# Performance work log

Measured on AMD Instinct MI355X. Metric: run time of the kernel, lower is better.

The kernel has to match this reference:

```python
import jax, jax.numpy as jnp
import numpy as np

NUM_ITEMS = 100000
N = NUM_ITEMS + 1
D = 64
H = 2
DH = D // H
NB = 2
DFF = 256
MAXLEN = 50
GNN_LAYERS = 2
L_SHORT, L_LONG = 10, 50


def layernorm(x, g, b, eps=1e-5):
    m = jnp.mean(x, axis=-1, keepdims=True)
    v = jnp.var(x, axis=-1, keepdims=True)
    return (x - m) / jnp.sqrt(v + eps) * g + b


def setup_inputs() -> dict:
    key = jax.random.key(0)
    ks = jax.random.split(key, 16)
    B, S, E = 1024, MAXLEN, 1_000_000
    s = 0.05
    inp = {}
    inp['seq'] = jax.random.randint(ks[0], (B, S), 0, N)
    inp['lengths'] = jax.random.randint(ks[1], (B,), 1, S + 1)
    inp['edge_index'] = jax.random.randint(ks[2], (2, E), 0, N)
    inp['edge_weight'] = jax.random.uniform(ks[3], (E,), dtype=jnp.float32)
    inp['bert_emb'] = jax.random.normal(ks[4], (N, D), dtype=jnp.float32) * s
    inp['gnn_emb'] = jax.random.normal(ks[5], (N, D), dtype=jnp.float32) * s
    inp['gnn_proj_w'] = jax.random.normal(ks[6], (D, D), dtype=jnp.float32) * s
    inp['gnn_proj_b'] = jnp.zeros((D,), jnp.float32)
    inp['pos_emb'] = jax.random.normal(ks[7], (MAXLEN, D), dtype=jnp.float32) * s
    inp['wq'] = jax.random.normal(ks[8], (NB, D, D), dtype=jnp.float32) * s
    inp['wk'] = jax.random.normal(ks[9], (NB, D, D), dtype=jnp.float32) * s
    inp['wv'] = jax.random.normal(ks[10], (NB, D, D), dtype=jnp.float32) * s
    inp['wo'] = jax.random.normal(ks[11], (NB, D, D), dtype=jnp.float32) * s
    inp['w1'] = jax.random.normal(ks[12], (NB, D, DFF), dtype=jnp.float32) * s
    inp['b1'] = jnp.zeros((NB, DFF), jnp.float32)
    inp['w2'] = jax.random.normal(ks[13], (NB, DFF, D), dtype=jnp.float32) * s
    inp['b2'] = jnp.zeros((NB, D), jnp.float32)
    inp['ln1_g'] = jnp.ones((NB, D), jnp.float32)
    inp['ln1_b'] = jnp.zeros((NB, D), jnp.float32)
    inp['ln2_g'] = jnp.ones((NB, D), jnp.float32)
    inp['ln2_b'] = jnp.zeros((NB, D), jnp.float32)
    inp['lnf_g'] = jnp.ones((D,), jnp.float32)
    inp['lnf_b'] = jnp.zeros((D,), jnp.float32)
    return inp


def reference(seq, lengths, edge_index, edge_weight, bert_emb, gnn_emb,
              gnn_proj_w, gnn_proj_b, pos_emb, wq, wk, wv, wo,
              w1, b1, w2, b2, ln1_g, ln1_b, ln2_g, ln2_b, lnf_g, lnf_b):
    B, S = seq.shape
    src, dst = edge_index[0], edge_index[1]

    # --- LightGCN: weighted neighbor aggregation, mean over layer outputs ---
    x = gnn_emb
    acc = gnn_emb
    for _ in range(GNN_LAYERS):
        x = jax.ops.segment_sum(x[src] * edge_weight[:, None], dst, num_segments=N)
        acc = acc + x
    gnn_out = acc / (GNN_LAYERS + 1)
    gnn_out = gnn_out @ gnn_proj_w + gnn_proj_b  # gnn_projection

    # --- Discrete fusion: per-user alpha from sequence length ---
    alpha = jnp.where(lengths <= L_SHORT, 0.3,
                      jnp.where(lengths >= L_LONG, 0.7, 0.5)).astype(bert_emb.dtype)
    # Gather-then-blend: identical math to materializing the full
    # [B, N, D] fused table and gathering rows by seq indices.
    seq_emb = (alpha[:, None, None] * bert_emb[seq]
               + (1.0 - alpha)[:, None, None] * gnn_out[seq])  # [B,S,D]

    x = seq_emb + pos_emb[None, :S, :]
    key_mask = (seq != 0)  # [B,S] key-side padding mask

    scale = 1.0 / np.sqrt(DH).astype(np.float32)
    for i in range(NB):
        q = (x @ wq[i]).reshape(B, S, H, DH)
        k = (x @ wk[i]).reshape(B, S, H, DH)
        v = (x @ wv[i]).reshape(B, S, H, DH)
        scores = jnp.einsum('bqhd,bkhd->bhqk', q, k) * scale
        scores = jnp.where(key_mask[:, None, None, :], scores, -1e9)
        attn = jax.nn.softmax(scores, axis=-1)
        ctx = jnp.einsum('bhqk,bkhd->bqhd', attn, v).reshape(B, S, D)
        x = layernorm(x + ctx @ wo[i], ln1_g[i], ln1_b[i])
        h = jax.nn.gelu(x @ w1[i] + b1[i])
        x = layernorm(x + h @ w2[i] + b2[i], ln2_g[i], ln2_b[i])

    x = layernorm(x, lnf_g, lnf_b)
    seq_repr = x[jnp.arange(B), lengths - 1]  # [B, D]
    return seq_repr
```

## Files before the change

kernel.cpp:

```cpp
#include <hip/hip_runtime.h>
#include <math.h>


typedef __attribute__((ext_vector_type(8))) short bf16x8;
typedef __attribute__((ext_vector_type(4))) float f32x4;

#define SD   64
#define SS   50
#define NBLK 2
#define PH   72
#define OVCAP 8192

__device__ __forceinline__ short f2b(float f) {
  union { __bf16 h; short s; } u;
  u.h = (__bf16)f;
  return u.s;
}
__device__ __forceinline__ float b2f(short s) {
  union { unsigned u; float f; } v;
  v.u = ((unsigned)(unsigned short)s) << 16;
  return v.f;
}
__device__ __forceinline__ unsigned packb(float a, float b) {
  union { __bf16 h; unsigned short s; } ua, ub;
  ua.h = (__bf16)a; ub.h = (__bf16)b;
  return (unsigned)ua.s | ((unsigned)ub.s << 16);
}
__device__ __forceinline__ float2 wred_sum2(float a, float b) {
#pragma unroll
  for (int o = 32; o > 0; o >>= 1) {
    a += __shfl_xor(a, o, 64);
    b += __shfl_xor(b, o, 64);
  }
  return make_float2(a, b);
}
__device__ __forceinline__ float gelu_fast(float x) {
  float u = 0.7978845608028654f * x * (1.0f + 0.044715f * x * x);
  float e = __expf(-2.f * u);
  return x * __builtin_amdgcn_rcpf(1.0f + e);
}

__device__ __forceinline__ bf16x8 ldB(const short* __restrict__ Wb, int tile, int lane) {
  return *(const bf16x8*)(Wb + ((size_t)tile * 64 + lane) * 8);
}

__device__ __forceinline__ void mm64(const short* A, const short* __restrict__ Wb,
                                     int arow, int quad, int lane, f32x4 o4[4]) {
  bf16x8 a0 = *(const bf16x8*)(A + arow * PH + quad * 8);
  bf16x8 a1 = *(const bf16x8*)(A + arow * PH + 32 + quad * 8);
#pragma unroll
  for (int nt = 0; nt < 4; ++nt) {
    f32x4 acc = {0.f, 0.f, 0.f, 0.f};
    acc = __builtin_amdgcn_mfma_f32_16x16x32_bf16(a0, ldB(Wb, 0 * 4 + nt, lane), acc, 0, 0, 0);
    acc = __builtin_amdgcn_mfma_f32_16x16x32_bf16(a1, ldB(Wb, 1 * 4 + nt, lane), acc, 0, 0, 0);
    o4[nt] = acc;
  }
}

__device__ __forceinline__ void ln_epilogue(f32x4 o4[4], short* xh,
                                            const float* __restrict__ g,
                                            const float* __restrict__ bta,
                                            const float* __restrict__ extrab,
                                            int mt, int quad, int c0) {
  float vals[4][4];
  float s1[4] = {0.f, 0.f, 0.f, 0.f}, s2[4] = {0.f, 0.f, 0.f, 0.f};
#pragma unroll
  for (int nt = 0; nt < 4; ++nt) {
    int c = nt * 16 + c0;
    float eb = extrab ? extrab[c] : 0.f;
#pragma unroll
    for (int r = 0; r < 4; ++r) {
      int row = mt * 16 + quad * 4 + r;
      float v = o4[nt][r] + b2f(xh[row * PH + c]) + eb;
      vals[nt][r] = v;
      s1[r] += v;
      s2[r] += v * v;
    }
  }
#pragma unroll
  for (int o = 1; o < 16; o <<= 1) {
#pragma unroll
    for (int r = 0; r < 4; ++r) {
      s1[r] += __shfl_xor(s1[r], o, 64);
      s2[r] += __shfl_xor(s2[r], o, 64);
    }
  }
  float mv[4], rv[4];
#pragma unroll
  for (int r = 0; r < 4; ++r) {
    float m = s1[r] * (1.f / 64);
    float var = fmaxf(s2[r] * (1.f / 64) - m * m, 0.f);
    mv[r] = m;
    rv[r] = rsqrtf(var + 1e-5f);
  }
#pragma unroll
  for (int nt = 0; nt < 4; ++nt) {
    int c = nt * 16 + c0;
    float gv = g[c], bv = bta[c];
#pragma unroll
    for (int r = 0; r < 4; ++r) {
      int row = mt * 16 + quad * 4 + r;
      xh[row * PH + c] = f2b((vals[nt][r] - mv[r]) * rv[r] * gv + bv);
    }
  }
}

__device__ __forceinline__ void prep_body(int tid,
    const float* __restrict__ pw, const float* __restrict__ wq,
    const float* __restrict__ wk, const float* __restrict__ wv,
    const float* __restrict__ wo, const float* __restrict__ w1,
    const float* __restrict__ w2,
    short* __restrict__ pwB, short* __restrict__ wqB,
    short* __restrict__ wkB, short* __restrict__ wvB,
    short* __restrict__ woB, short* __restrict__ w1B,
    short* __restrict__ w2B) {
  int lane = tid & 63;
  int tile = tid >> 6;
  const float* W; short* out; int K, N, base;
  if (tile < 8)        { W = pw; out = pwB; K = 64;  N = 64;  base = 0; }
  else if (tile < 24)  { W = wq; out = wqB; K = 64;  N = 64;  base = 8; }
  else if (tile < 40)  { W = wk; out = wkB; K = 64;  N = 64;  base = 24; }
  else if (tile < 56)  { W = wv; out = wvB; K = 64;  N = 64;  base = 40; }
  else if (tile < 72)  { W = wo; out = woB; K = 64;  N = 64;  base = 56; }
  else if (tile < 136) { W = w1; out = w1B; K = 64;  N = 256; base = 72; }
  else if (tile < 200) { W = w2; out = w2B; K = 256; N = 64;  base = 136; }
  else return;
  int lt = tile - base;
  int KT = K / 32, NT = N / 16;
  int nt = lt % NT; lt /= NT;
  int kt = lt % KT; lt /= KT;
  int m = lt;
  const float* Wm = W + (size_t)m * K * N;
  int kbase = kt * 32 + ((lane >> 4) * 8);
  int n = nt * 16 + (lane & 15);
  short v[8];
#pragma unroll
  for (int j = 0; j < 8; ++j) v[j] = f2b(Wm[(size_t)(kbase + j) * N + n]);
  *(bf16x8*)(out + ((size_t)(tile - base) * 64 + lane) * 8) = *(bf16x8*)v;
}

__global__ void prep_zero(const float* __restrict__ pw, const float* __restrict__ wq,
                          const float* __restrict__ wk, const float* __restrict__ wv,
                          const float* __restrict__ wo, const float* __restrict__ w1,
                          const float* __restrict__ w2,
                          short* __restrict__ pwB, short* __restrict__ wqB,
                          short* __restrict__ wkB, short* __restrict__ wvB,
                          short* __restrict__ woB, short* __restrict__ w1B,
                          short* __restrict__ w2B,
                          const float* __restrict__ gnn, unsigned* __restrict__ gnnh,
                          int n32, int* __restrict__ cntp, int cntn,
                          int* __restrict__ flagsw, int nfw, int* __restrict__ ovcnt) {
  int tid = blockIdx.x * blockDim.x + threadIdx.x;
  int NT = gridDim.x * blockDim.x;
  prep_body(tid, pw, wq, wk, wv, wo, w1, w2, pwB, wqB, wkB, wvB, woB, w1B, w2B);
  for (int i = tid; i < cntn; i += NT) cntp[i] = 0;
  for (int i = tid; i < nfw; i += NT) flagsw[i] = 0;
  if (tid < 4) ovcnt[tid] = 0;
  for (int i = tid; i < n32; i += NT) {
    float2 f = ((const float2*)gnn)[i];
    gnnh[i] = packb(f.x, f.y);
  }
}

__global__ void gnn_build(const int* __restrict__ src, const int* __restrict__ dst,
                          const float* __restrict__ ew, int* __restrict__ cntp,
                          int cs, int cap, int2* __restrict__ ep,
                          int4* __restrict__ ov, int* __restrict__ ovcnt,
                          const int* __restrict__ seq,
                          unsigned char* __restrict__ flags, int BS,
                          int E, int Nn) {
  int tid = blockIdx.x * 256 + threadIdx.x;
  for (int i = tid; i < BS; i += gridDim.x * 256) flags[seq[i]] = 1;
  int p = blockIdx.x & 7;
  int sub = blockIdx.x >> 3;
  int nsub = gridDim.x >> 3;
  int lo = (int)(((long)p * Nn) >> 3);
  int hi = (int)(((long)(p + 1) * Nn) >> 3);
  for (int e = sub * 256 + threadIdx.x; e < E; e += nsub * 256) {
    int d = dst[e];
    if (d >= lo && d < hi) {
      int pos = atomicAdd(&cntp[d * cs], 1);
      if (pos < cap) {
        ep[(size_t)d * cap + pos] = make_int2(src[e], __float_as_int(ew[e]));
      } else {
        int oi = atomicAdd(ovcnt, 1);
        if (oi < OVCAP) ov[oi] = make_int4(d, src[e], __float_as_int(ew[e]), 0);
      }
    }
  }
}

__device__ __forceinline__ void gather_accum(float a[8], uint4 p, float w) {
  a[0] += b2f((short)(p.x & 0xFFFF)) * w;
  a[1] += b2f((short)(p.x >> 16)) * w;
  a[2] += b2f((short)(p.y & 0xFFFF)) * w;
  a[3] += b2f((short)(p.y >> 16)) * w;
  a[4] += b2f((short)(p.z & 0xFFFF)) * w;
  a[5] += b2f((short)(p.z >> 16)) * w;
  a[6] += b2f((short)(p.w & 0xFFFF)) * w;
  a[7] += b2f((short)(p.w >> 16)) * w;
}
__device__ __forceinline__ void gather_accum_idx(float a[8],
    const unsigned* __restrict__ tab, int srcn, float w, int g) {
  uint4 p = *(const uint4*)(tab + (size_t)srcn * 32 + g * 4);
  gather_accum(a, p, w);
}

__device__ __forceinline__ void gather_core(float a[8], int n, int slot, int g,
    const unsigned* __restrict__ tab, const int* __restrict__ cntp, int cs, int cap,
    const int2* __restrict__ ep, const int4* __restrict__ ov,
    const int* __restrict__ ovcnt, int Nn) {
  int deg = cntp[n * cs];
  int2 e[4];
#pragma unroll
  for (int b = 0; b < 4; ++b)
    e[b] = ep[(size_t)n * cap + slot + 4 * b];
  uint4 r[4];
#pragma unroll
  for (int b = 0; b < 4; ++b) {
    int s = min(max(e[b].x, 0), Nn - 1);
    r[b] = *(const uint4*)(tab + (size_t)s * 32 + g * 4);
  }
  int end = min(deg, cap);
#pragma unroll
  for (int b = 0; b < 4; ++b)
    if (slot + 4 * b < end) gather_accum(a, r[b], __int_as_float(e[b].y));
  for (int i = slot + 16; i < end; i += 4) {
    int2 ee = ep[(size_t)n * cap + i];
    gather_accum_idx(a, tab, min(max(ee.x, 0), Nn - 1), __int_as_float(ee.y), g);
  }
  if (deg > cap && slot == 0) {
    int ovn = min(max(*ovcnt, 0), OVCAP);
    for (int i = 0; i < ovn; ++i) {
      int4 eo = ov[i];
      if (eo.x == n) gather_accum_idx(a, tab, min(max(eo.y, 0), Nn - 1),
                                      __int_as_float(eo.z), g);
    }
  }
}

__global__ void gnn_gather1(const unsigned* __restrict__ xinh,
                            const int* __restrict__ cntp, int cs, int cap,
                            const int2* __restrict__ ep, const int4* __restrict__ ov,
                            const int* __restrict__ ovcnt,
                            unsigned* __restrict__ xouth, int Nn) {
  int n = blockIdx.x * 8 + (threadIdx.x >> 5);
  if (n >= Nn) return;
  int l32 = threadIdx.x & 31;
  int slot = l32 >> 3, g = l32 & 7;
  float a[8] = {0.f, 0.f, 0.f, 0.f, 0.f, 0.f, 0.f, 0.f};
  gather_core(a, n, slot, g, xinh, cntp, cs, cap, ep, ov, ovcnt, Nn);
#pragma unroll
  for (int o = 8; o < 32; o <<= 1)
#pragma unroll
    for (int j = 0; j < 8; ++j) a[j] += __shfl_xor(a[j], o, 64);
  if (slot == 0) {
    uint4 o4;
    o4.x = packb(a[0], a[1]);
    o4.y = packb(a[2], a[3]);
    o4.z = packb(a[4], a[5]);
    o4.w = packb(a[6], a[7]);
    *(uint4*)(xouth + (size_t)n * 32 + g * 4) = o4;
  }
}

__global__ void gnn_gather_avg(const unsigned* __restrict__ x1h,
                               const int* __restrict__ cntp, int cs, int cap,
                               const int2* __restrict__ ep, const int4* __restrict__ ov,
                               const int* __restrict__ ovcnt,
                               const float* __restrict__ gnn,
                               unsigned* __restrict__ avgh, int Nn,
                               const unsigned char* __restrict__ flags) {
  int n = blockIdx.x * 8 + (threadIdx.x >> 5);
  if (n >= Nn) return;
  if (!flags[n]) return;
  int l32 = threadIdx.x & 31;
  int slot = l32 >> 3, g = l32 & 7;
  float a[8] = {0.f, 0.f, 0.f, 0.f, 0.f, 0.f, 0.f, 0.f};
  gather_core(a, n, slot, g, x1h, cntp, cs, cap, ep, ov, ovcnt, Nn);
#pragma unroll
  for (int o = 8; o < 32; o <<= 1)
#pragma unroll
    for (int j = 0; j < 8; ++j) a[j] += __shfl_xor(a[j], o, 64);
  if (slot == 0) {
    uint4 own = *(const uint4*)(x1h + (size_t)n * 32 + g * 4);
    float4 g0 = *(const float4*)(gnn + (size_t)n * 64 + g * 8);
    float4 g1 = *(const float4*)(gnn + (size_t)n * 64 + g * 8 + 4);
    float v0 = (g0.x + b2f((short)(own.x & 0xFFFF)) + a[0]) * (1.f / 3.f);
    float v1 = (g0.y + b2f((short)(own.x >> 16)) + a[1]) * (1.f / 3.f);
    float v2 = (g0.z + b2f((short)(own.y & 0xFFFF)) + a[2]) * (1.f / 3.f);
    float v3 = (g0.w + b2f((short)(own.y >> 16)) + a[3]) * (1.f / 3.f);
    float v4 = (g1.x + b2f((short)(own.z & 0xFFFF)) + a[4]) * (1.f / 3.f);
    float v5 = (g1.y + b2f((short)(own.z >> 16)) + a[5]) * (1.f / 3.f);
    float v6 = (g1.z + b2f((short)(own.w & 0xFFFF)) + a[6]) * (1.f / 3.f);
    float v7 = (g1.w + b2f((short)(own.w >> 16)) + a[7]) * (1.f / 3.f);
    uint4 o4;
    o4.x = packb(v0, v1);
    o4.y = packb(v2, v3);
    o4.z = packb(v4, v5);
    o4.w = packb(v6, v7);
    *(uint4*)(avgh + (size_t)n * 32 + g * 4) = o4;
  }
}

__global__ void prep_only(const float* __restrict__ pw, const float* __restrict__ wq,
                          const float* __restrict__ wk, const float* __restrict__ wv,
                          const float* __restrict__ wo, const float* __restrict__ w1,
                          const float* __restrict__ w2,
                          short* __restrict__ pwB, short* __restrict__ wqB,
                          short* __restrict__ wkB, short* __restrict__ wvB,
                          short* __restrict__ woB, short* __restrict__ w1B,
                          short* __restrict__ w2B) {
  prep_body(blockIdx.x * blockDim.x + threadIdx.x,
            pw, wq, wk, wv, wo, w1, w2, pwB, wqB, wkB, wvB, woB, w1B, w2B);
}
__global__ void zero_ws(int* __restrict__ p, int n) {
  int tid = blockIdx.x * blockDim.x + threadIdx.x;
  int NT = gridDim.x * blockDim.x;
  for (int i = tid; i < n; i += NT) p[i] = 0;
}
__global__ void gnn_scatter(const float* __restrict__ xin,
                            const int* __restrict__ src,
                            const int* __restrict__ dst,
                            const float* __restrict__ ew,
                            float* __restrict__ xout, int E) {
  int gid = blockIdx.x * blockDim.x + threadIdx.x;
  int e = gid >> 6;
  int d = gid & 63;
  if (e >= E) return;
  atomicAdd(&xout[(size_t)dst[e] * SD + d], xin[(size_t)src[e] * SD + d] * ew[e]);
}
__global__ void avg_from_f32(const float* __restrict__ gnn, const float* __restrict__ g1,
                             const float* __restrict__ g2, unsigned* __restrict__ avgh,
                             int n32) {
  int i = blockIdx.x * blockDim.x + threadIdx.x;
  if (i >= n32) return;
  float2 a = ((const float2*)gnn)[i];
  float2 b = ((const float2*)g1)[i];
  float2 c = ((const float2*)g2)[i];
  avgh[i] = packb((a.x + b.x + c.x) * (1.f / 3.f), (a.y + b.y + c.y) * (1.f / 3.f));
}

__global__ __launch_bounds__(256, 3)
void seq_transformer(const int* __restrict__ seq, const int* __restrict__ lengths,
                     const float* __restrict__ bert, const short* __restrict__ avgh,
                     const float* __restrict__ pbias, const float* __restrict__ pos,
                     const short* __restrict__ pwB, const short* __restrict__ wqB,
                     const short* __restrict__ wkB, const short* __restrict__ wvB,
                     const short* __restrict__ woB, const short* __restrict__ w1B,
                     const short* __restrict__ w2B,
                     const float* __restrict__ b1, const float* __restrict__ b2,
                     const float* __restrict__ ln1g, const float* __restrict__ ln1b,
                     const float* __restrict__ ln2g, const float* __restrict__ ln2b,
                     const float* __restrict__ lnfg, const float* __restrict__ lnfb,
                     float* __restrict__ out) {
  __shared__ short xh[64 * PH];
  __shared__ short qh[64 * PH];
  __shared__ short kh[64 * PH];
  __shared__ short vt[64 * PH];
  __shared__ short s0[64 * PH];
  __shared__ int   sidx[64];

  const int t = threadIdx.x;
  const int lane = t & 63;
  const int mt = t >> 6;
  const int quad = lane >> 4;
  const int c0 = lane & 15;
  const int b = blockIdx.x;
  const int arow = mt * 16 + c0;

  if (t < 64) sidx[t] = (t < SS) ? seq[b * SS + t] : 0;
  __syncthreads();

  const int len = lengths[b];
  const float alpha = (len <= 10) ? 0.3f : ((len >= 50) ? 0.7f : 0.5f);
  const float isq = 0.17677669529663687f;

  float kbias[4];
#pragma unroll
  for (int nt = 0; nt < 4; ++nt) {
    int key = nt * 16 + c0;
    kbias[nt] = (key < SS && sidx[key] != 0) ? 0.f : -1e9f;
  }

#pragma unroll
  for (int ir = 0; ir < 16; ++ir) {
    int s = mt * 16 + ir;
    short v = 0;
    if (s < SS) v = avgh[(size_t)sidx[s] * SD + lane];
    qh[s * PH + lane] = v;
  }

  {
    f32x4 o4[4];
    mm64(qh, pwB, arow, quad, lane, o4);
#pragma unroll
    for (int nt = 0; nt < 4; ++nt) {
      int c = nt * 16 + c0;
      float pbv = pbias[c];
#pragma unroll
      for (int r = 0; r < 4; ++r) {
        int row = mt * 16 + quad * 4 + r;
        short ov8 = 0;
        if (row < SS) {
          float g = o4[nt][r] + pbv;
          float xv = alpha * bert[(size_t)sidx[row] * SD + c] +
                     (1.f - alpha) * g + pos[row * SD + c];
          ov8 = f2b(xv);
        }
        xh[row * PH + c] = ov8;
      }
    }
  }

#pragma unroll 1
  for (int blk = 0; blk < NBLK; ++blk) {
    const short* Wq = wqB + blk * 4096;
    const short* Wk = wkB + blk * 4096;
    const short* Wv = wvB + blk * 4096;
    const short* Wo = woB + blk * 4096;
    const short* W1 = w1B + blk * 16384;
    const short* W2 = w2B + blk * 16384;

    __syncthreads();

    {
      f32x4 o4[4];
      mm64(xh, Wq, arow, quad, lane, o4);
#pragma unroll
      for (int nt = 0; nt < 4; ++nt) {
        int c = nt * 16 + c0;
#pragma unroll
        for (int r = 0; r < 4; ++r) qh[(mt * 16 + quad * 4 + r) * PH + c] = f2b(o4[nt][r]);
      }
      mm64(xh, Wk, arow, quad, lane, o4);
#pragma unroll
      for (int nt = 0; nt < 4; ++nt) {
        int c = nt * 16 + c0;
#pragma unroll
        for (int r = 0; r < 4; ++r) kh[(mt * 16 + quad * 4 + r) * PH + c] = f2b(o4[nt][r]);
      }
      mm64(xh, Wv, arow, quad, lane, o4);
#pragma unroll
      for (int nt = 0; nt < 4; ++nt) {
        int dim = nt * 16 + c0;
        unsigned p0 = packb(o4[nt][0], o4[nt][1]);
        unsigned p1 = packb(o4[nt][2], o4[nt][3]);
        *(uint2*)(vt + (size_t)dim * PH + mt * 16 + quad * 4) = make_uint2(p0, p1);
      }
    }
    __syncthreads();

#pragma unroll
    for (int h = 0; h < 2; ++h) {
      {
        bf16x8 aq = *(const bf16x8*)(qh + arow * PH + h * 32 + quad * 8);
        float p[4][4];
        float mx[4], sm[4];
#pragma unroll
        for (int nt = 0; nt < 4; ++nt) {
          int key = nt * 16 + c0;
          bf16x8 bk = *(const bf16x8*)(kh + key * PH + h * 32 + quad * 8);
          f32x4 acc = {0.f, 0.f, 0.f, 0.f};
          acc = __builtin_amdgcn_mfma_f32_16x16x32_bf16(aq, bk, acc, 0, 0, 0);
#pragma unroll
          for (int r = 0; r < 4; ++r) p[nt][r] = fmaf(acc[r], isq, kbias[nt]);
        }
#pragma unroll
        for (int r = 0; r < 4; ++r)
          mx[r] = fmaxf(fmaxf(p[0][r], p[1][r]), fmaxf(p[2][r], p[3][r]));
#pragma unroll
        for (int o = 1; o < 16; o <<= 1)
#pragma unroll
          for (int r = 0; r < 4; ++r) mx[r] = fmaxf(mx[r], __shfl_xor(mx[r], o, 64));
#pragma unroll
        for (int r = 0; r < 4; ++r) sm[r] = 0.f;
#pragma unroll
        for (int nt = 0; nt < 4; ++nt)
#pragma unroll
          for (int r = 0; r < 4; ++r) {
            float e = __expf(p[nt][r] - mx[r]);
            p[nt][r] = e;
            sm[r] += e;
          }
#pragma unroll
        for (int o = 1; o < 16; o <<= 1)
#pragma unroll
          for (int r = 0; r < 4; ++r) sm[r] += __shfl_xor(sm[r], o, 64);
#pragma unroll
        for (int r = 0; r < 4; ++r) {
          float inv = __builtin_amdgcn_rcpf(sm[r]);
          int q = mt * 16 + quad * 4 + r;
#pragma unroll
          for (int nt = 0; nt < 4; ++nt)
            s0[q * PH + nt * 16 + c0] = f2b(p[nt][r] * inv);
        }
      }
      {
        bf16x8 a0 = *(const bf16x8*)(s0 + arow * PH + quad * 8);
        bf16x8 a1 = *(const bf16x8*)(s0 + arow * PH + 32 + quad * 8);
#pragma unroll
        for (int nt = 0; nt < 2; ++nt) {
          int dim = h * 32 + nt * 16 + c0;
          bf16x8 b0 = *(const bf16x8*)(vt + (size_t)dim * PH + quad * 8);
          bf16x8 b1v = *(const bf16x8*)(vt + (size_t)dim * PH + 32 + quad * 8);
          f32x4 acc = {0.f, 0.f, 0.f, 0.f};
          acc = __builtin_amdgcn_mfma_f32_16x16x32_bf16(a0, b0, acc, 0, 0, 0);
          acc = __builtin_amdgcn_mfma_f32_16x16x32_bf16(a1, b1v, acc, 0, 0, 0);
#pragma unroll
          for (int r = 0; r < 4; ++r)
            qh[(mt * 16 + quad * 4 + r) * PH + dim] = f2b(acc[r]);
        }
      }
    }

    {
      f32x4 o4[4];
      mm64(qh, Wo, arow, quad, lane, o4);
      ln_epilogue(o4, xh, ln1g + blk * SD, ln1b + blk * SD, nullptr, mt, quad, c0);
    }

    f32x4 facc[4];
#pragma unroll
    for (int nt = 0; nt < 4; ++nt) facc[nt] = (f32x4){0.f, 0.f, 0.f, 0.f};
#pragma unroll 1
    for (int c = 0; c < 4; ++c) {
      {
        bf16x8 a0 = *(const bf16x8*)(xh + arow * PH + quad * 8);
        bf16x8 a1 = *(const bf16x8*)(xh + arow * PH + 32 + quad * 8);
#pragma unroll
        for (int nt = 0; nt < 4; ++nt) {
          int ntg = c * 4 + nt;
          f32x4 acc = {0.f, 0.f, 0.f, 0.f};
          acc = __builtin_amdgcn_mfma_f32_16x16x32_bf16(a0, ldB(W1, 0 * 16 + ntg, lane), acc, 0, 0, 0);
          acc = __builtin_amdgcn_mfma_f32_16x16x32_bf16(a1, ldB(W1, 1 * 16 + ntg, lane), acc, 0, 0, 0);
          int cc = nt * 16 + c0;
          float b1v = b1[blk * 256 + c * 64 + cc];
#pragma unroll
          for (int r = 0; r < 4; ++r)
            qh[(mt * 16 + quad * 4 + r) * PH + cc] = f2b(gelu_fast(acc[r] + b1v));
        }
      }
      {
        bf16x8 a0 = *(const bf16x8*)(qh + arow * PH + quad * 8);
        bf16x8 a1 = *(const bf16x8*)(qh + arow * PH + 32 + quad * 8);
#pragma unroll
        for (int nt = 0; nt < 4; ++nt) {
          facc[nt] = __builtin_amdgcn_mfma_f32_16x16x32_bf16(a0, ldB(W2, (2 * c) * 4 + nt, lane), facc[nt], 0, 0, 0);
          facc[nt] = __builtin_amdgcn_mfma_f32_16x16x32_bf16(a1, ldB(W2, (2 * c + 1) * 4 + nt, lane), facc[nt], 0, 0, 0);
        }
      }
    }

    ln_epilogue(facc, xh, ln2g + blk * SD, ln2b + blk * SD, b2 + blk * SD, mt, quad, c0);
  }
  __syncthreads();

  if (mt == 0) {
    int sl = len - 1;
    float val = b2f(xh[sl * PH + lane]);
    float2 ss = wred_sum2(val, val * val);
    float m = ss.x * (1.f / 64);
    float var = fmaxf(ss.y * (1.f / 64) - m * m, 0.f);
    float rs = rsqrtf(var + 1e-5f);
    out[b * SD + lane] = (val - m) * rs * lnfg[lane] + lnfb[lane];
  }
}

extern "C" void kernel_launch(void* const* d_in, const int* in_sizes, int n_in,
                              void* d_out, int out_size, void* d_ws, size_t ws_size,
                              hipStream_t stream) {
  const int*   seq   = (const int*)d_in[0];
  const int*   lens  = (const int*)d_in[1];
  const int*   ei    = (const int*)d_in[2];
  const float* ew    = (const float*)d_in[3];
  const float* bert  = (const float*)d_in[4];
  const float* gnn   = (const float*)d_in[5];
  const float* pw    = (const float*)d_in[6];
  const float* pb    = (const float*)d_in[7];
  const float* pos   = (const float*)d_in[8];
  const float* wq    = (const float*)d_in[9];
  const float* wk    = (const float*)d_in[10];
  const float* wv    = (const float*)d_in[11];
  const float* wo    = (const float*)d_in[12];
  const float* w1    = (const float*)d_in[13];
  const float* b1    = (const float*)d_in[14];
  const float* w2    = (const float*)d_in[15];
  const float* b2    = (const float*)d_in[16];
  const float* ln1g  = (const float*)d_in[17];
  const float* ln1b  = (const float*)d_in[18];
  const float* ln2g  = (const float*)d_in[19];
  const float* ln2b  = (const float*)d_in[20];
  const float* lnfg  = (const float*)d_in[21];
  const float* lnfb  = (const float*)d_in[22];
  float* out = (float*)d_out;

  const int E = in_sizes[2] / 2;
  const int B = in_sizes[0] / SS;
  const int N = in_sizes[4] / SD;
  const int BS = B * SS;

  const int* esrc = ei;
  const int* edst = ei + E;

  const int Nr = (N + 1023) & ~1023;
  const int NF = (N + 15) & ~15;
  const int n32 = N * 32;

  short* pwB; short* wqB; short* wkB; short* wvB; short* woB; short* w1B; short* w2B;
  unsigned* gnnh; unsigned* g1xh; unsigned* avgh;
  int* cntp; unsigned char* flags; int* ovcnt; int4* ov; int2* ep;
  int cs = 4, cap = 32;
  auto layout = [&](int cstride, int capv) -> size_t {
    pwB = (short*)d_ws;
    wqB = pwB + 4096;
    wkB = wqB + 8192;
    wvB = wkB + 8192;
    woB = wvB + 8192;
    w1B = woB + 8192;
    w2B = w1B + 32768;
    gnnh = (unsigned*)(w2B + 32768);
    g1xh = gnnh + (size_t)N * 32;
    cntp = (int*)(g1xh + (size_t)N * 32);
    flags = (unsigned char*)(cntp + (size_t)Nr * cstride);
    ovcnt = (int*)(flags + NF);
    ov = (int4*)(ovcnt + 4);
    ep = (int2*)(ov + OVCAP);
    avgh = gnnh;
    return (size_t)((char*)(ep + (size_t)N * capv) - (char*)d_ws);
  };
  size_t need = layout(4, 32); cs = 4; cap = 32;
  if (need > ws_size) { need = layout(1, 32); cs = 1; cap = 32; }
  if (need > ws_size) { need = layout(1, 24); cs = 1; cap = 24; }

  float* g1x = (float*)ep;
  float* g2x = g1x + (size_t)N * SD;
  size_t need_fb = (size_t)((char*)(g2x + (size_t)N * SD) - (char*)d_ws);

  if (need <= ws_size) {
    const int cntn = Nr * cs;
    prep_zero<<<1024, 256, 0, stream>>>(pw, wq, wk, wv, wo, w1, w2,
                                        pwB, wqB, wkB, wvB, woB, w1B, w2B,
                                        gnn, gnnh, n32, cntp, cntn,
                                        (int*)flags, NF / 4, ovcnt);
    gnn_build<<<1024, 256, 0, stream>>>(esrc, edst, ew, cntp, cs, cap, ep,
                                        ov, ovcnt, seq, flags, BS, E, N);
    const int nb = (N + 7) / 8;
    gnn_gather1<<<nb, 256, 0, stream>>>(gnnh, cntp, cs, cap, ep, ov, ovcnt,
                                        g1xh, N);
    gnn_gather_avg<<<nb, 256, 0, stream>>>(g1xh, cntp, cs, cap, ep, ov, ovcnt,
                                           gnn, (unsigned*)avgh, N, flags);
  } else if (ws_size >= need_fb) {
    prep_only<<<50, 256, 0, stream>>>(pw, wq, wk, wv, wo, w1, w2,
                                      pwB, wqB, wkB, wvB, woB, w1B, w2B);
    zero_ws<<<1024, 256, 0, stream>>>((int*)g1x, 2 * N * SD);
    const long total = (long)E * 64;
    const int sblocks = (int)((total + 255) / 256);
    gnn_scatter<<<sblocks, 256, 0, stream>>>(gnn, esrc, edst, ew, g1x, E);
    gnn_scatter<<<sblocks, 256, 0, stream>>>(g1x, esrc, edst, ew, g2x, E);
    avg_from_f32<<<(n32 + 255) / 256, 256, 0, stream>>>(gnn, g1x, g2x,
                                                        (unsigned*)avgh, n32);
  }

  seq_transformer<<<B, 256, 0, stream>>>(
      seq, lens, bert, (const short*)avgh, pb, pos,
      pwB, wqB, wkB, wvB, woB, w1B, w2B,
      b1, b2, ln1g, ln1b, ln2g, ln2b, lnfg, lnfb, out);
}
```

Before: 308.5 us.

## Move weight prep and bf16 packing into edge build; grid-stride gather kernels

Splits zeroing into a small standalone kernel and folds the weight bf16 conversion and GNN table packing into the edge-bucketing kernel, which now launches 2048 blocks. The two gather kernels become persistent grid-stride loops over nodes with fixed 2048-block grids instead of one block per 8 nodes. Gather loads for unused neighbor slots are skipped rather than clamped and issued. This aims to cut per-block launch overhead and wasted loads, at the cost of making the build kernel heavier and possibly reducing latency hiding in the gather loops.

Measured after the change: 307.2 us. No clear change (-0.4%).

```diff
diff --git a/kernel.cpp b/kernel.cpp
--- a/kernel.cpp
+++ b/kernel.cpp
@@ -139,38 +139,41 @@
   *(bf16x8*)(out + ((size_t)(tile - base) * 64 + lane) * 8) = *(bf16x8*)v;
 }
 
-__global__ void prep_zero(const float* __restrict__ pw, const float* __restrict__ wq,
+__global__ void zero_only(int* __restrict__ cntp, int cntn,
+                          int* __restrict__ flagsw, int nfw,
+                          int* __restrict__ ovcnt) {
+  int tid = blockIdx.x * blockDim.x + threadIdx.x;
+  int NT = gridDim.x * blockDim.x;
+  for (int i = tid; i < cntn; i += NT) cntp[i] = 0;
+  for (int i = tid; i < nfw; i += NT) flagsw[i] = 0;
+  if (tid < 4) ovcnt[tid] = 0;
+}
+
+__global__ void gnn_build(const int* __restrict__ src, const int* __restrict__ dst,
+                          const float* __restrict__ ew, int* __restrict__ cntp,
+                          int cs, int cap, int2* __restrict__ ep,
+                          int4* __restrict__ ov, int* __restrict__ ovcnt,
+                          const int* __restrict__ seq,
+                          unsigned char* __restrict__ flags, int BS,
+                          int E, int Nn,
+                          const float* __restrict__ gnn, unsigned* __restrict__ gnnh,
+                          int n32,
+                          const float* __restrict__ pw, const float* __restrict__ wq,
                           const float* __restrict__ wk, const float* __restrict__ wv,
                           const float* __restrict__ wo, const float* __restrict__ w1,
                           const float* __restrict__ w2,
                           short* __restrict__ pwB, short* __restrict__ wqB,
                           short* __restrict__ wkB, short* __restrict__ wvB,
                           short* __restrict__ woB, short* __restrict__ w1B,
-                          short* __restrict__ w2B,
-                          const float* __restrict__ gnn, unsigned* __restrict__ gnnh,
-                          int n32, int* __restrict__ cntp, int cntn,
-                          int* __restrict__ flagsw, int nfw, int* __restrict__ ovcnt) {
-  int tid = blockIdx.x * blockDim.x + threadIdx.x;
-  int NT = gridDim.x * blockDim.x;
+                          short* __restrict__ w2B) {
+  int tid = blockIdx.x * 256 + threadIdx.x;
+  int NT = gridDim.x * 256;
   prep_body(tid, pw, wq, wk, wv, wo, w1, w2, pwB, wqB, wkB, wvB, woB, w1B, w2B);
-  for (int i = tid; i < cntn; i += NT) cntp[i] = 0;
-  for (int i = tid; i < nfw; i += NT) flagsw[i] = 0;
-  if (tid < 4) ovcnt[tid] = 0;
   for (int i = tid; i < n32; i += NT) {
     float2 f = ((const float2*)gnn)[i];
     gnnh[i] = packb(f.x, f.y);
   }
-}
-
-__global__ void gnn_build(const int* __restrict__ src, const int* __restrict__ dst,
-                          const float* __restrict__ ew, int* __restrict__ cntp,
-                          int cs, int cap, int2* __restrict__ ep,
-                          int4* __restrict__ ov, int* __restrict__ ovcnt,
-                          const int* __restrict__ seq,
-                          unsigned char* __restrict__ flags, int BS,
-                          int E, int Nn) {
-  int tid = blockIdx.x * 256 + threadIdx.x;
-  for (int i = tid; i < BS; i += gridDim.x * 256) flags[seq[i]] = 1;
+  for (int i = tid; i < BS; i += NT) flags[seq[i]] = 1;
   int p = blockIdx.x & 7;
   int sub = blockIdx.x >> 3;
   int nsub = gridDim.x >> 3;
@@ -215,13 +218,15 @@
 #pragma unroll
   for (int b = 0; b < 4; ++b)
     e[b] = ep[(size_t)n * cap + slot + 4 * b];
-  uint4 r[4];
+  int end = min(deg, cap);
+  uint4 r[4] = {};
 #pragma unroll
   for (int b = 0; b < 4; ++b) {
-    int s = min(max(e[b].x, 0), Nn - 1);
-    r[b] = *(const uint4*)(tab + (size_t)s * 32 + g * 4);
-  }
-  int end = min(deg, cap);
+    if (slot + 4 * b < end) {
+      int s = min(max(e[b].x, 0), Nn - 1);
+      r[b] = *(const uint4*)(tab + (size_t)s * 32 + g * 4);
+    }
+  }
 #pragma unroll
   for (int b = 0; b < 4; ++b)
     if (slot + 4 * b < end) gather_accum(a, r[b], __int_as_float(e[b].y));
@@ -244,23 +249,23 @@
                             const int2* __restrict__ ep, const int4* __restrict__ ov,
                             const int* __restrict__ ovcnt,
                             unsigned* __restrict__ xouth, int Nn) {
-  int n = blockIdx.x * 8 + (threadIdx.x >> 5);
-  if (n >= Nn) return;
   int l32 = threadIdx.x & 31;
   int slot = l32 >> 3, g = l32 & 7;
-  float a[8] = {0.f, 0.f, 0.f, 0.f, 0.f, 0.f, 0.f, 0.f};
-  gather_core(a, n, slot, g, xinh, cntp, cs, cap, ep, ov, ovcnt, Nn);
-#pragma unroll
-  for (int o = 8; o < 32; o <<= 1)
-#pragma unroll
-    for (int j = 0; j < 8; ++j) a[j] += __shfl_xor(a[j], o, 64);
-  if (slot == 0) {
-    uint4 o4;
-    o4.x = packb(a[0], a[1]);
-    o4.y = packb(a[2], a[3]);
-    o4.z = packb(a[4], a[5]);
-    o4.w = packb(a[6], a[7]);
-    *(uint4*)(xouth + (size_t)n * 32 + g * 4) = o4;
+  for (int n = blockIdx.x * 8 + (threadIdx.x >> 5); n < Nn; n += gridDim.x * 8) {
+    float a[8] = {0.f, 0.f, 0.f, 0.f, 0.f, 0.f, 0.f, 0.f};
+    gather_core(a, n, slot, g, xinh, cntp, cs, cap, ep, ov, ovcnt, Nn);
+#pragma unroll
+    for (int o = 8; o < 32; o <<= 1)
+#pragma unroll
+      for (int j = 0; j < 8; ++j) a[j] += __shfl_xor(a[j], o, 64);
+    if (slot == 0) {
+      uint4 o4;
+      o4.x = packb(a[0], a[1]);
+      o4.y = packb(a[2], a[3]);
+      o4.z = packb(a[4], a[5]);
+      o4.w = packb(a[6], a[7]);
+      *(uint4*)(xouth + (size_t)n * 32 + g * 4) = o4;
+    }
   }
 }
 
@@ -271,35 +276,35 @@
                                const float* __restrict__ gnn,
                                unsigned* __restrict__ avgh, int Nn,
                                const unsigned char* __restrict__ flags) {
-  int n = blockIdx.x * 8 + (threadIdx.x >> 5);
-  if (n >= Nn) return;
-  if (!flags[n]) return;
   int l32 = threadIdx.x & 31;
   int slot = l32 >> 3, g = l32 & 7;
-  float a[8] = {0.f, 0.f, 0.f, 0.f, 0.f, 0.f, 0.f, 0.f};
-  gather_core(a, n, slot, g, x1h, cntp, cs, cap, ep, ov, ovcnt, Nn);
-#pragma unroll
-  for (int o = 8; o < 32; o <<= 1)
-#pragma unroll
-    for (int j = 0; j < 8; ++j) a[j] += __shfl_xor(a[j], o, 64);
-  if (slot == 0) {
-    uint4 own = *(const uint4*)(x1h + (size_t)n * 32 + g * 4);
-    float4 g0 = *(const float4*)(gnn + (size_t)n * 64 + g * 8);
-    float4 g1 = *(const float4*)(gnn + (size_t)n * 64 + g * 8 + 4);
-    float v0 = (g0.x + b2f((short)(own.x & 0xFFFF)) + a[0]) * (1.f / 3.f);
-    float v1 = (g0.y + b2f((short)(own.x >> 16)) + a[1]) * (1.f / 3.f);
-    float v2 = (g0.z + b2f((short)(own.y & 0xFFFF)) + a[2]) * (1.f / 3.f);
-    float v3 = (g0.w + b2f((short)(own.y >> 16)) + a[3]) * (1.f / 3.f);
-    float v4 = (g1.x + b2f((short)(own.z & 0xFFFF)) + a[4]) * (1.f / 3.f);
-    float v5 = (g1.y + b2f((short)(own.z >> 16)) + a[5]) * (1.f / 3.f);
-    float v6 = (g1.z + b2f((short)(own.w & 0xFFFF)) + a[6]) * (1.f / 3.f);
-    float v7 = (g1.w + b2f((short)(own.w >> 16)) + a[7]) * (1.f / 3.f);
-    uint4 o4;
-    o4.x = packb(v0, v1);
-    o4.y = packb(v2, v3);
-    o4.z = packb(v4, v5);
-    o4.w = packb(v6, v7);
-    *(uint4*)(avgh + (size_t)n * 32 + g * 4) = o4;
+  for (int n = blockIdx.x * 8 + (threadIdx.x >> 5); n < Nn; n += gridDim.x * 8) {
+    if (!flags[n]) continue;
+    float a[8] = {0.f, 0.f, 0.f, 0.f, 0.f, 0.f, 0.f, 0.f};
+    gather_core(a, n, slot, g, x1h, cntp, cs, cap, ep, ov, ovcnt, Nn);
+#pragma unroll
+    for (int o = 8; o < 32; o <<= 1)
+#pragma unroll
+      for (int j = 0; j < 8; ++j) a[j] += __shfl_xor(a[j], o, 64);
+    if (slot == 0) {
+      uint4 own = *(const uint4*)(x1h + (size_t)n * 32 + g * 4);
+      float4 g0 = *(const float4*)(gnn + (size_t)n * 64 + g * 8);
+      float4 g1 = *(const float4*)(gnn + (size_t)n * 64 + g * 8 + 4);
+      float v0 = (g0.x + b2f((short)(own.x & 0xFFFF)) + a[0]) * (1.f / 3.f);
+      float v1 = (g0.y + b2f((short)(own.x >> 16)) + a[1]) * (1.f / 3.f);
+      float v2 = (g0.z + b2f((short)(own.y & 0xFFFF)) + a[2]) * (1.f / 3.f);
+      float v3 = (g0.w + b2f((short)(own.y >> 16)) + a[3]) * (1.f / 3.f);
+      float v4 = (g1.x + b2f((short)(own.z & 0xFFFF)) + a[4]) * (1.f / 3.f);
+      float v5 = (g1.y + b2f((short)(own.z >> 16)) + a[5]) * (1.f / 3.f);
+      float v6 = (g1.z + b2f((short)(own.w & 0xFFFF)) + a[6]) * (1.f / 3.f);
+      float v7 = (g1.w + b2f((short)(own.w >> 16)) + a[7]) * (1.f / 3.f);
+      uint4 o4;
+      o4.x = packb(v0, v1);
+      o4.y = packb(v2, v3);
+      o4.z = packb(v4, v5);
+      o4.w = packb(v6, v7);
+      *(uint4*)(avgh + (size_t)n * 32 + g * 4) = o4;
+    }
   }
 }
 
@@ -639,17 +644,16 @@
 
   if (need <= ws_size) {
     const int cntn = Nr * cs;
-    prep_zero<<<1024, 256, 0, stream>>>(pw, wq, wk, wv, wo, w1, w2,
-                                        pwB, wqB, wkB, wvB, woB, w1B, w2B,
-                                        gnn, gnnh, n32, cntp, cntn,
-                                        (int*)flags, NF / 4, ovcnt);
-    gnn_build<<<1024, 256, 0, stream>>>(esrc, edst, ew, cntp, cs, cap, ep,
-                                        ov, ovcnt, seq, flags, BS, E, N);
-    const int nb = (N + 7) / 8;
-    gnn_gather1<<<nb, 256, 0, stream>>>(gnnh, cntp, cs, cap, ep, ov, ovcnt,
-                                        g1xh, N);
-    gnn_gather_avg<<<nb, 256, 0, stream>>>(g1xh, cntp, cs, cap, ep, ov, ovcnt,
-                                           gnn, (unsigned*)avgh, N, flags);
+    zero_only<<<256, 256, 0, stream>>>(cntp, cntn, (int*)flags, NF / 4, ovcnt);
+    gnn_build<<<2048, 256, 0, stream>>>(esrc, edst, ew, cntp, cs, cap, ep,
+                                        ov, ovcnt, seq, flags, BS, E, N,
+                                        gnn, gnnh, n32,
+                                        pw, wq, wk, wv, wo, w1, w2,
+                                        pwB, wqB, wkB, wvB, woB, w1B, w2B);
+    gnn_gather1<<<2048, 256, 0, stream>>>(gnnh, cntp, cs, cap, ep, ov, ovcnt,
+                                          g1xh, N);
+    gnn_gather_avg<<<2048, 256, 0, stream>>>(g1xh, cntp, cs, cap, ep, ov, ovcnt,
+                                             gnn, (unsigned*)avgh, N, flags);
   } else if (ws_size >= need_fb) {
     prep_only<<<50, 256, 0, stream>>>(pw, wq, wk, wv, wo, w1, w2,
                                       pwB, wqB, wkB, wvB, woB, w1B, w2B);
```
